# Kernel tuning notes

Hardware: AMD Instinct MI355X
Metric: run time of the kernel (lower is better)

## Reference

```python
import jax, jax.numpy as jnp
import numpy as np
import itertools, math

M_MODES = 10
N_PHOT = 5
IN_MODES = np.array([0, 2, 4, 6, 8])  # input_state = [1,0,1,0,...], 5 photons
INV_SQRT2 = 0.7071067811865476

# Fock output bases (lexicographic ordering)
ROWS_NB = np.array(list(itertools.combinations(range(M_MODES), N_PHOT)), np.int32)          # [252,5] no-bunching
ROWS_B = np.array(list(itertools.combinations_with_replacement(range(M_MODES), N_PHOT)), np.int32)  # [2002,5] bunched

def _norms(rows):
    out = []
    for r in rows:
        c = np.bincount(r, minlength=M_MODES)
        out.append(float(np.prod([math.factorial(int(v)) for v in c])))
    return np.array(out, np.float32)

NORM_NB = _norms(ROWS_NB)  # all ones
NORM_B = _norms(ROWS_B)

# Glynn sign vectors for n=5 permanents (delta_0 fixed to +1): [16,5]
_D = np.array(list(itertools.product([1.0, -1.0], repeat=N_PHOT - 1)), np.float32)
DELTAS = np.concatenate([np.ones((_D.shape[0], 1), np.float32), _D], axis=1)
DSIGNS = np.prod(DELTAS, axis=1)


def _mzi(t1, t2):
    # BS // PS(t1) // BS // PS(t2); BS = (1/sqrt2)[[1,i],[i,1]], PS on first mode of pair
    B = jnp.array([[1.0, 1.0j], [1.0j, 1.0]], dtype=jnp.complex64) * INV_SQRT2
    e1 = jnp.exp(1j * t1)
    e2 = jnp.exp(1j * t2)
    M1 = B * jnp.stack([e1, jnp.ones_like(e1)])[:, None]   # PS(t1) @ BS
    M2 = B @ M1                                            # BS @ ...
    return M2 * jnp.stack([e2, jnp.ones_like(e2)])[:, None]  # PS(t2) @ ...


def interferometer(phases):
    """Rectangular (Clements) mesh on 10 modes with 45 MZIs; phases [45,2] -> U [10,10] complex."""
    Ts = jax.vmap(lambda p: _mzi(p[0], p[1]))(phases)  # [45,2,2]
    U = jnp.eye(M_MODES, dtype=jnp.complex64)
    k = 0
    for layer in range(M_MODES):
        for p in range(layer % 2, M_MODES - 1, 2):
            U = U.at[p:p + 2, :].set(Ts[k] @ U[p:p + 2, :])
            k += 1
    return U


def batched_permanent(Ms):
    """Glynn formula for [...,5,5] complex matrices."""
    D = jnp.asarray(DELTAS, dtype=Ms.dtype)       # [16,5]
    s = jnp.asarray(DSIGNS, dtype=Ms.dtype)       # [16]
    rowsum = jnp.einsum('di,...ij->...dj', D, Ms)  # [...,16,5]
    return jnp.einsum('d,...d->...', s, jnp.prod(rowsum, axis=-1)) / (2 ** (N_PHOT - 1))


def fock_probs(U, rows, norm):
    """U [B,10,10]; rows [K,5] output-mode indices (with repetition for bunching); norm [K]."""
    M = U[:, rows][..., IN_MODES]        # [B,K,5,5]
    perm = batched_permanent(M)          # [B,K]
    return (jnp.abs(perm) ** 2) / jnp.asarray(norm)


def _forward(x, W_down, b_down, phases_l1, phases_r1, phases_lf, phases_rf, W_out, b_out):
    h = (x @ W_down + b_down) / jnp.pi                 # downscale + DivideByPi -> [B,10]
    WL1 = interferometer(phases_l1)
    WR1 = interferometer(phases_r1)
    U1 = jnp.einsum('mk,bk,kn->bmn', WR1, jnp.exp(1j * h), WL1)  # WR @ diag(e^{i phi}) @ WL
    e1 = fock_probs(U1, ROWS_NB, NORM_NB)              # [B,252], no_bunching=True
    # final circuit: 252 px phase shifters round-robin over 10 modes -> phases add per mode
    Bsz = e1.shape[0]
    pad = jnp.pad(e1, ((0, 0), (0, 260 - 252)))
    phi2 = pad.reshape(Bsz, 26, M_MODES).sum(axis=1)   # [B,10]
    WLF = interferometer(phases_lf)
    WRF = interferometer(phases_rf)
    UF = jnp.einsum('mk,bk,kn->bmn', WRF, jnp.exp(1j * phi2), WLF)
    probs = fock_probs(UF, ROWS_B, NORM_B)             # [B,2002], bunched Fock states
    return probs @ W_out + b_out                       # [B,num_classes]


def setup_inputs() -> dict:
    key = jax.random.key(0)
    ks = jax.random.split(key, 9)
    two_pi = 2.0 * np.pi
    return {
        'x': jax.random.normal(ks[0], (128, 784), dtype=jnp.float32),
        'W_down': jax.random.normal(ks[1], (784, 10), dtype=jnp.float32) * 0.05,
        'b_down': jax.random.normal(ks[2], (10,), dtype=jnp.float32) * 0.05,
        'phases_l1': jax.random.uniform(ks[3], (45, 2), dtype=jnp.float32) * two_pi,
        'phases_r1': jax.random.uniform(ks[4], (45, 2), dtype=jnp.float32) * two_pi,
        'phases_lf': jax.random.uniform(ks[5], (45, 2), dtype=jnp.float32) * two_pi,
        'phases_rf': jax.random.uniform(ks[6], (45, 2), dtype=jnp.float32) * two_pi,
        'W_out': jax.random.normal(ks[7], (2002, 10), dtype=jnp.float32) * 0.02,
        'b_out': jax.random.normal(ks[8], (10,), dtype=jnp.float32) * 0.02,
    }


def reference(x, W_down, b_down, phases_l1, phases_r1, phases_lf, phases_rf, W_out, b_out):
    return _forward(x, W_down, b_down, phases_l1, phases_r1, phases_lf, phases_rf, W_out, b_out)
```

## Files before the change

### kernel.cpp

```cpp
#include <hip/hip_runtime.h>
#include <math.h>


#define PI_F 3.14159265358979323846f

__constant__ float FACTF[6] = {1.f, 1.f, 2.f, 6.f, 24.f, 120.f};

__device__ __forceinline__ float2 cmul(float2 a, float2 b) {
  return make_float2(fmaf(a.x, b.x, -a.y * b.y), fmaf(a.x, b.y, a.y * b.x));
}
__device__ __forceinline__ float2 cadd(float2 a, float2 b) {
  return make_float2(a.x + b.x, a.y + b.y);
}
__device__ __forceinline__ float2 cscale(float2 a, float s) {
  return make_float2(a.x * s, a.y * s);
}
__device__ __forceinline__ float2 imul(float2 a) {
  return make_float2(-a.y, a.x);
}

__device__ __forceinline__ void unrank5f(int rank, float cnt0, float m0,
                                         int c[5]) {
  float r = (float)rank;
  float cnt = cnt0, m = m0, j = 4.f;
  int x = 0;
#pragma unroll
  for (int i = 0; i < 5; i++) {
    while (r >= cnt) {
      r -= cnt;
      cnt = cnt * (m - j) / m;
      m -= 1.f;
      x++;
    }
    c[i] = x;
    cnt = cnt * j / m;
    m -= 1.f;
    j -= 1.f;
    x++;
  }
}

__device__ __forceinline__ float2 prod5(const float2 rs[5]) {
  return cmul(cmul(cmul(rs[0], rs[1]), cmul(rs[2], rs[3])), rs[4]);
}

__device__ __forceinline__ float2 perm5(const float2 M[5][5]) {
  float2 rs[5];
#pragma unroll
  for (int j = 0; j < 5; j++) {
    rs[j] = M[0][j];
#pragma unroll
    for (int i = 1; i < 5; i++) rs[j] = cadd(rs[j], M[i][j]);
  }
  float2 acc = prod5(rs);
#pragma unroll
  for (int t = 1; t < 16; t++) {
    const int g = t ^ (t >> 1);
    const int bit = (t & 1) ? 0 : ((t & 2) ? 1 : ((t & 4) ? 2 : 3));
    const int i = bit + 1;
    const float step = ((g >> bit) & 1) ? -2.0f : 2.0f;
#pragma unroll
    for (int j = 0; j < 5; j++) {
      rs[j].x = fmaf(step, M[i][j].x, rs[j].x);
      rs[j].y = fmaf(step, M[i][j].y, rs[j].y);
    }
    float2 p = prod5(rs);
    const float s = (__popc(g) & 1) ? -1.0f : 1.0f;
    acc.x = fmaf(s, p.x, acc.x);
    acc.y = fmaf(s, p.y, acc.y);
  }
  return make_float2(acc.x * (1.0f / 16.0f), acc.y * (1.0f / 16.0f));
}

__global__ __launch_bounds__(256) void k_all(
    const float* __restrict__ x, const float* __restrict__ Wd,
    const float* __restrict__ bd, const float* __restrict__ ph_l1,
    const float* __restrict__ ph_r1, const float* __restrict__ ph_lf,
    const float* __restrict__ ph_rf, const float* __restrict__ Wout,
    const float* __restrict__ bout, float* __restrict__ out) {
  const int b = blockIdx.x >> 3, chunk = blockIdx.x & 7;
  const int tid = threadIdx.x;

  __shared__ float2 T[4][45][4];
  __shared__ float2 Ui[4][100];
  __shared__ float2 Ub[100];
  __shared__ float  e1s[252];
  __shared__ float  red[4][10];
  __shared__ float2 v[10];

  float hacc[10];
#pragma unroll
  for (int c = 0; c < 10; c++) hacc[c] = 0.f;
  for (int i = tid; i < 784; i += 256) {
    float xv = x[b * 784 + i];
    const float* w = Wd + i * 10;
#pragma unroll
    for (int c = 0; c < 10; c++) hacc[c] = fmaf(xv, w[c], hacc[c]);
  }

  if (tid < 180) {
    const int which = tid / 45, m = tid % 45;
    const float* ph = (which == 0) ? ph_l1
                    : (which == 1) ? ph_r1
                    : (which == 2) ? ph_lf : ph_rf;
    float t1 = ph[m * 2 + 0], t2 = ph[m * 2 + 1];
    float s1, c1, s2, c2;
    sincosf(t1, &s1, &c1);
    sincosf(t2, &s2, &c2);
    float2 e2  = make_float2(c2, s2);
    float2 e1m = make_float2(c1 - 1.f, s1);
    float2 e1p = make_float2(c1 + 1.f, s1);
    T[which][m][0] = cscale(cmul(e2, e1m), 0.5f);
    T[which][m][1] = cscale(cmul(e2, imul(e1p)), 0.5f);
    T[which][m][2] = cscale(imul(e1p), 0.5f);
    T[which][m][3] = make_float2(0.5f * (1.f - c1), -0.5f * s1);
  }

  {
    const int lane = tid & 63, wave = tid >> 6;
#pragma unroll
    for (int c = 0; c < 10; c++) {
      float r = hacc[c];
#pragma unroll
      for (int d = 32; d > 0; d >>= 1) r += __shfl_down(r, d);
      if (lane == 0) red[wave][c] = r;
    }
  }
  __syncthreads();

  if (tid < 40) {
    const int which = tid / 10, n = tid % 10;
    float2 u[10];
#pragma unroll
    for (int m = 0; m < 10; m++)
      u[m] = make_float2(m == n ? 1.f : 0.f, 0.f);
    int kb = 0;
#pragma unroll
    for (int layer = 0; layer < 10; layer++) {
      const int start = layer & 1;
      const int npairs = 5 - start;
      for (int pi = 0; pi < npairs; pi++) {
        const int p = start + 2 * pi;
        const int k = kb + pi;
        float2 u0 = u[p], u1 = u[p + 1];
        u[p]     = cadd(cmul(T[which][k][0], u0), cmul(T[which][k][1], u1));
        u[p + 1] = cadd(cmul(T[which][k][2], u0), cmul(T[which][k][3], u1));
      }
      kb += npairs;
    }
#pragma unroll
    for (int m = 0; m < 10; m++) Ui[which][m * 10 + n] = u[m];
  } else if (tid >= 64 && tid < 74) {
    const int c = tid - 64;
    float s = red[0][c] + red[1][c] + red[2][c] + red[3][c] + bd[c];
    s *= (1.0f / PI_F);
    float sn, cs;
    sincosf(s, &sn, &cs);
    v[c] = make_float2(cs, sn);
  }
  __syncthreads();

  if (tid < 100) {
    const int m = tid / 10, n = tid % 10;
    float2 acc = make_float2(0.f, 0.f);
#pragma unroll
    for (int k = 0; k < 10; k++)
      acc = cadd(acc, cmul(cmul(Ui[1][m * 10 + k], v[k]), Ui[0][k * 10 + n]));
    Ub[tid] = acc;
  }
  __syncthreads();

  if (tid < 252) {
    int c[5];
    unrank5f(tid, 126.f, 9.f, c);
    float2 M[5][5];
#pragma unroll
    for (int i = 0; i < 5; i++)
#pragma unroll
      for (int j = 0; j < 5; j++) M[i][j] = Ub[c[i] * 10 + 2 * j];
    float2 p = perm5(M);
    e1s[tid] = p.x * p.x + p.y * p.y;
  }
  __syncthreads();

  if (tid < 10) {
    float s = 0.f;
    for (int idx = tid; idx < 252; idx += 10) s += e1s[idx];
    float sn, cs;
    sincosf(s, &sn, &cs);
    v[tid] = make_float2(cs, sn);
  }
  __syncthreads();

  if (tid < 100) {
    const int m = tid / 10, n = tid % 10;
    float2 acc = make_float2(0.f, 0.f);
#pragma unroll
    for (int k = 0; k < 10; k++)
      acc = cadd(acc, cmul(cmul(Ui[3][m * 10 + k], v[k]), Ui[2][k * 10 + n]));
    Ub[tid] = acc;
  }
  __syncthreads();

  float acc[10];
#pragma unroll
  for (int c = 0; c < 10; c++) acc[c] = 0.f;
  const int k = chunk * 256 + tid;
  if (k < 2002) {
    int c5[5];
    unrank5f(k, 715.f, 13.f, c5);
    int modes[5];
#pragma unroll
    for (int i = 0; i < 5; i++) modes[i] = c5[i] - i;
    float2 M[5][5];
#pragma unroll
    for (int i = 0; i < 5; i++)
#pragma unroll
      for (int j = 0; j < 5; j++) M[i][j] = Ub[modes[i] * 10 + 2 * j];
    float2 p = perm5(M);
    float norm = 1.f;
    int run = 1;
#pragma unroll
    for (int i = 1; i < 5; i++) {
      if (modes[i] == modes[i - 1]) run++;
      else { norm *= FACTF[run]; run = 1; }
    }
    norm *= FACTF[run];
    const float pv = (p.x * p.x + p.y * p.y) / norm;
    const float2* w2 = (const float2*)Wout + k * 5;
#pragma unroll
    for (int c = 0; c < 5; c++) {
      float2 w = w2[c];
      acc[2 * c + 0] = pv * w.x;
      acc[2 * c + 1] = pv * w.y;
    }
  }

  {
    const int lane = tid & 63, wave = tid >> 6;
#pragma unroll
    for (int c = 0; c < 10; c++) {
      float r = acc[c];
#pragma unroll
      for (int d = 32; d > 0; d >>= 1) r += __shfl_down(r, d);
      if (lane == 0) red[wave][c] = r;
    }
  }
  __syncthreads();
  if (tid < 10) {
    float s = red[0][tid] + red[1][tid] + red[2][tid] + red[3][tid];
    if (chunk == 0) s += bout[tid];
    atomicAdd(&out[b * 10 + tid], s);
  }
}

extern "C" void kernel_launch(void* const* d_in, const int* in_sizes, int n_in,
                              void* d_out, int out_size, void* d_ws,
                              size_t ws_size, hipStream_t stream) {
  const float* x    = (const float*)d_in[0];
  const float* Wd   = (const float*)d_in[1];
  const float* bd   = (const float*)d_in[2];
  const float* pl1  = (const float*)d_in[3];
  const float* pr1  = (const float*)d_in[4];
  const float* plf  = (const float*)d_in[5];
  const float* prf  = (const float*)d_in[6];
  const float* Wout = (const float*)d_in[7];
  const float* bout = (const float*)d_in[8];
  float* out = (float*)d_out;

  hipMemsetAsync(out, 0, (size_t)out_size * sizeof(float), stream);
  k_all<<<1024, 256, 0, stream>>>(x, Wd, bd, pl1, pr1, plf, prf, Wout, bout,
                                  out);
}
```

Baseline: 101.7 us.

## Split fused kernel into per-sample prefix kernel and permanent-sum kernel

Before, each of the 8 chunk blocks per sample recomputed the whole prefix: downsampling, four interferometers, the 252 no-bunching permanents and the second unitary. That prefix now runs once per sample in a separate 128-block kernel, which writes the final unitary to workspace and initializes the output with the bias. A second 1024-block kernel loads the unitary and computes the 2002 bunched permanents. The change also uses fast __sincosf, fully unrolls the MZI loop and computes the factorial normalization arithmetically. The trade-off is an extra launch and a workspace round trip, plus slightly lower trig precision.

Measured after the change: 90.25 us. -11.3%, faster.

```diff
diff --git a/kernel.cpp b/kernel.cpp
--- a/kernel.cpp
+++ b/kernel.cpp
@@ -3,8 +3,6 @@
 
 
 #define PI_F 3.14159265358979323846f
-
-__constant__ float FACTF[6] = {1.f, 1.f, 2.f, 6.f, 24.f, 120.f};
 
 __device__ __forceinline__ float2 cmul(float2 a, float2 b) {
   return make_float2(fmaf(a.x, b.x, -a.y * b.y), fmaf(a.x, b.y, a.y * b.x));
@@ -72,14 +70,13 @@
   return make_float2(acc.x * (1.0f / 16.0f), acc.y * (1.0f / 16.0f));
 }
 
-__global__ __launch_bounds__(256) void k_all(
+__global__ __launch_bounds__(256) void k_prefix(
     const float* __restrict__ x, const float* __restrict__ Wd,
     const float* __restrict__ bd, const float* __restrict__ ph_l1,
     const float* __restrict__ ph_r1, const float* __restrict__ ph_lf,
-    const float* __restrict__ ph_rf, const float* __restrict__ Wout,
-    const float* __restrict__ bout, float* __restrict__ out) {
-  const int b = blockIdx.x >> 3, chunk = blockIdx.x & 7;
-  const int tid = threadIdx.x;
+    const float* __restrict__ ph_rf, const float* __restrict__ bout,
+    float2* __restrict__ UFws, float* __restrict__ out) {
+  const int b = blockIdx.x, tid = threadIdx.x;
 
   __shared__ float2 T[4][45][4];
   __shared__ float2 Ui[4][100];
@@ -105,8 +102,8 @@
                     : (which == 2) ? ph_lf : ph_rf;
     float t1 = ph[m * 2 + 0], t2 = ph[m * 2 + 1];
     float s1, c1, s2, c2;
-    sincosf(t1, &s1, &c1);
-    sincosf(t2, &s2, &c2);
+    __sincosf(t1, &s1, &c1);
+    __sincosf(t2, &s2, &c2);
     float2 e2  = make_float2(c2, s2);
     float2 e1m = make_float2(c1 - 1.f, s1);
     float2 e1p = make_float2(c1 + 1.f, s1);
@@ -139,12 +136,15 @@
     for (int layer = 0; layer < 10; layer++) {
       const int start = layer & 1;
       const int npairs = 5 - start;
-      for (int pi = 0; pi < npairs; pi++) {
-        const int p = start + 2 * pi;
-        const int k = kb + pi;
-        float2 u0 = u[p], u1 = u[p + 1];
-        u[p]     = cadd(cmul(T[which][k][0], u0), cmul(T[which][k][1], u1));
-        u[p + 1] = cadd(cmul(T[which][k][2], u0), cmul(T[which][k][3], u1));
+#pragma unroll
+      for (int pi = 0; pi < 5; pi++) {
+        if (pi < npairs) {
+          const int p = start + 2 * pi;
+          const int k = kb + pi;
+          float2 u0 = u[p], u1 = u[p + 1];
+          u[p]     = cadd(cmul(T[which][k][0], u0), cmul(T[which][k][1], u1));
+          u[p + 1] = cadd(cmul(T[which][k][2], u0), cmul(T[which][k][3], u1));
+        }
       }
       kb += npairs;
     }
@@ -155,7 +155,7 @@
     float s = red[0][c] + red[1][c] + red[2][c] + red[3][c] + bd[c];
     s *= (1.0f / PI_F);
     float sn, cs;
-    sincosf(s, &sn, &cs);
+    __sincosf(s, &sn, &cs);
     v[c] = make_float2(cs, sn);
   }
   __syncthreads();
@@ -187,7 +187,7 @@
     float s = 0.f;
     for (int idx = tid; idx < 252; idx += 10) s += e1s[idx];
     float sn, cs;
-    sincosf(s, &sn, &cs);
+    __sincosf(s, &sn, &cs);
     v[tid] = make_float2(cs, sn);
   }
   __syncthreads();
@@ -198,14 +198,27 @@
 #pragma unroll
     for (int k = 0; k < 10; k++)
       acc = cadd(acc, cmul(cmul(Ui[3][m * 10 + k], v[k]), Ui[2][k * 10 + n]));
-    Ub[tid] = acc;
-  }
+    UFws[b * 100 + tid] = acc;
+  }
+  if (tid < 10) out[b * 10 + tid] = bout[tid];
+}
+
+__global__ __launch_bounds__(256) void k_perms(const float2* __restrict__ UFws,
+                                               const float* __restrict__ Wout,
+                                               float* __restrict__ out) {
+  const int b = blockIdx.x >> 3, chunk = blockIdx.x & 7;
+  const int tid = threadIdx.x;
+  const int k = chunk * 256 + tid;
+  __shared__ float2 U[100];
+  __shared__ float red[4][10];
+  if (tid < 50)
+    ((float4*)U)[tid] = ((const float4*)(UFws + b * 100))[tid];
   __syncthreads();
 
   float acc[10];
 #pragma unroll
   for (int c = 0; c < 10; c++) acc[c] = 0.f;
-  const int k = chunk * 256 + tid;
+
   if (k < 2002) {
     int c5[5];
     unrank5f(k, 715.f, 13.f, c5);
@@ -216,16 +229,14 @@
 #pragma unroll
     for (int i = 0; i < 5; i++)
 #pragma unroll
-      for (int j = 0; j < 5; j++) M[i][j] = Ub[modes[i] * 10 + 2 * j];
+      for (int j = 0; j < 5; j++) M[i][j] = U[modes[i] * 10 + 2 * j];
     float2 p = perm5(M);
-    float norm = 1.f;
-    int run = 1;
+    float norm = 1.f, cnt = 1.f;
 #pragma unroll
     for (int i = 1; i < 5; i++) {
-      if (modes[i] == modes[i - 1]) run++;
-      else { norm *= FACTF[run]; run = 1; }
-    }
-    norm *= FACTF[run];
+      cnt = (modes[i] == modes[i - 1]) ? cnt + 1.f : 1.f;
+      norm *= cnt;
+    }
     const float pv = (p.x * p.x + p.y * p.y) / norm;
     const float2* w2 = (const float2*)Wout + k * 5;
 #pragma unroll
@@ -236,20 +247,17 @@
     }
   }
 
-  {
-    const int lane = tid & 63, wave = tid >> 6;
-#pragma unroll
-    for (int c = 0; c < 10; c++) {
-      float r = acc[c];
-#pragma unroll
-      for (int d = 32; d > 0; d >>= 1) r += __shfl_down(r, d);
-      if (lane == 0) red[wave][c] = r;
-    }
+  const int lane = tid & 63, wave = tid >> 6;
+#pragma unroll
+  for (int c = 0; c < 10; c++) {
+    float r = acc[c];
+#pragma unroll
+    for (int d = 32; d > 0; d >>= 1) r += __shfl_down(r, d);
+    if (lane == 0) red[wave][c] = r;
   }
   __syncthreads();
   if (tid < 10) {
     float s = red[0][tid] + red[1][tid] + red[2][tid] + red[3][tid];
-    if (chunk == 0) s += bout[tid];
     atomicAdd(&out[b * 10 + tid], s);
   }
 }
@@ -268,7 +276,9 @@
   const float* bout = (const float*)d_in[8];
   float* out = (float*)d_out;
 
-  hipMemsetAsync(out, 0, (size_t)out_size * sizeof(float), stream);
-  k_all<<<1024, 256, 0, stream>>>(x, Wd, bd, pl1, pr1, plf, prf, Wout, bout,
-                                  out);
-}
+  float2* UFws = (float2*)d_ws;
+
+  k_prefix<<<128, 256, 0, stream>>>(x, Wd, bd, pl1, pr1, plf, prf, bout, UFws,
+                                    out);
+  k_perms<<<1024, 256, 0, stream>>>(UFws, Wout, out);
+}
```
